# Optimization experiments

Measured on AMD Instinct MI355X. Metric: run time of the kernel, lower is better.

## Reference

```python
import jax, jax.numpy as jnp
import numpy as np

V = 50000

def _spmm(edge_vals, edge_row, edge_col, x):
    # sparse (V,V) @ dense (V,F) via gather + segment_sum
    return jax.ops.segment_sum(edge_vals[:, None] * x[edge_col], edge_row, num_segments=V)

def setup_inputs() -> dict:
    key = jax.random.key(0)
    ks = jax.random.split(key, 6)
    B, Cin, Cout, K, E = 4, 128, 128, 4, 800000
    x = jax.random.normal(ks[0], (B, Cin, V), dtype=jnp.float32)
    edge_row = jax.random.randint(ks[1], (E,), 0, V, dtype=jnp.int32)
    edge_col = jax.random.randint(ks[2], (E,), 0, V, dtype=jnp.int32)
    edge_vals = jax.random.normal(ks[3], (E,), dtype=jnp.float32) * 0.05
    std = np.sqrt(2.0 / (Cin * K)).astype(np.float32)
    weights = jax.random.normal(ks[4], (K, Cin, Cout), dtype=jnp.float32) * std
    biases = jnp.full((Cout,), 0.01, dtype=jnp.float32)
    return {"x": x, "edge_row": edge_row, "edge_col": edge_col,
            "edge_vals": edge_vals, "weights": weights, "biases": biases}

def reference(x, edge_row, edge_col, edge_vals, weights, biases):
    B, Cin, Vv = x.shape
    K = weights.shape[0]
    # (B,Cin,V) -> (V, B*Cin)
    x0 = jnp.transpose(x, (2, 0, 1)).reshape(Vv, B * Cin)
    xs = [x0]
    if K > 1:
        x1 = _spmm(edge_vals, edge_row, edge_col, x0)
        xs.append(x1)
        for _ in range(2, K):
            x2 = 2.0 * _spmm(edge_vals, edge_row, edge_col, x1) - x0
            xs.append(x2)
            x0, x1 = x1, x2
    xk = jnp.stack(xs, 0).reshape(K, Vv, B, Cin)
    # tensordot over (K, Cin): (K,V,B,Cin) x (K,Cin,Cout) -> (V,B,Cout)
    out = jnp.einsum('kvbc,kco->vbo', xk, weights)
    out = out + biases
    # permute (V,B,Cout) -> (B,Cout,V)
    return jnp.transpose(out, (1, 2, 0))
```

## Files before the change

kernel.cpp:

```cpp
#include <hip/hip_runtime.h>

#define V_N   50000
#define B_N   4
#define C_IN  128
#define C_OUT 128
#define E_N   800000
#define F_N   512
#define M_TOT 200000

typedef unsigned short ushort_t;
typedef __attribute__((ext_vector_type(8))) short short8;
typedef __attribute__((ext_vector_type(4))) float f32x4;

__device__ __forceinline__ float bf_lo(unsigned u) { return __uint_as_float(u << 16); }
__device__ __forceinline__ float bf_hi(unsigned u) { return __uint_as_float(u & 0xFFFF0000u); }
__device__ __forceinline__ ushort_t f2bf(float f) {
    unsigned u = __float_as_uint(f);
    u += 0x7FFFu + ((u >> 16) & 1u);
    return (ushort_t)(u >> 16);
}

__global__ __launch_bounds__(256) void k_transpose_in(const float* __restrict__ x,
                                                      ushort_t* __restrict__ x0) {
    __shared__ float tile[32][33];
    int vb = blockIdx.x * 32;
    int fb = blockIdx.y * 32;
    int tx = threadIdx.x, ty = threadIdx.y;
#pragma unroll
    for (int i = 0; i < 32; i += 8) {
        int f = fb + ty + i, v = vb + tx;
        float val = 0.f;
        if (v < V_N) val = x[(size_t)f * V_N + v];
        tile[ty + i][tx] = val;
    }
    __syncthreads();
#pragma unroll
    for (int i = 0; i < 32; i += 8) {
        int v = vb + ty + i, f = fb + tx;
        if (v < V_N) x0[(size_t)v * F_N + f] = f2bf(tile[tx][ty + i]);
    }
}

__global__ __launch_bounds__(256) void k_hist(const int* __restrict__ row,
                                              int* __restrict__ counts) {
    int e = blockIdx.x * blockDim.x + threadIdx.x;
    if (e < E_N) atomicAdd(&counts[row[e]], 1);
}

__global__ __launch_bounds__(1024) void k_scan(const int* __restrict__ counts,
                                               int* __restrict__ row_ptr,
                                               int* __restrict__ next) {
    __shared__ int sums[1024];
    int t = threadIdx.x;
    const int CH = (V_N + 1023) / 1024;
    int base = t * CH;
    int s = 0;
    for (int i = 0; i < CH; i++) {
        int idx = base + i;
        if (idx < V_N) s += counts[idx];
    }
    sums[t] = s;
    __syncthreads();
    for (int off = 1; off < 1024; off <<= 1) {
        int v = (t >= off) ? sums[t - off] : 0;
        __syncthreads();
        sums[t] += v;
        __syncthreads();
    }
    int run = (t == 0) ? 0 : sums[t - 1];
    for (int i = 0; i < CH; i++) {
        int idx = base + i;
        if (idx < V_N) {
            row_ptr[idx] = run;
            next[idx]    = run;
            run += counts[idx];
        }
    }
    if (t == 1023) row_ptr[V_N] = run;
}

__global__ __launch_bounds__(256) void k_scatter(const int* __restrict__ row,
                                                 const int* __restrict__ col,
                                                 const float* __restrict__ vals,
                                                 int* __restrict__ next,
                                                 int2* __restrict__ edges) {
    int e = blockIdx.x * blockDim.x + threadIdx.x;
    if (e < E_N) {
        int r = row[e];
        int pos = atomicAdd(&next[r], 1);
        edges[pos] = make_int2(col[e], __float_as_int(vals[e]));
    }
}

__global__ __launch_bounds__(256) void k_wprep(const float* __restrict__ W,
                                               ushort_t* __restrict__ Wt) {
    int i = blockIdx.x * 256 + threadIdx.x;
    int k = i >> 14, c = (i >> 7) & 127, o = i & 127;
    Wt[((size_t)k * 128 + o) * 128 + c] = f2bf(W[i]);
}

__global__ __launch_bounds__(256) void k_spmm_bf16(const int* __restrict__ row_ptr,
                                                   const int2* __restrict__ edges,
                                                   const ushort_t* __restrict__ src,
                                                   const ushort_t* __restrict__ prev,
                                                   ushort_t* __restrict__ dst,
                                                   float alpha, float beta,
                                                   int has_prev) {
    int lane = threadIdx.x & 63;
    int g = blockIdx.x * 4 + (threadIdx.x >> 6);
    int r = g >> 1;
    int h = g & 1;
    int e0 = row_ptr[r], e1 = row_ptr[r + 1];
    float a0 = 0.f, a1 = 0.f, a2 = 0.f, a3 = 0.f;
    const ushort_t* sp = src + h * 256 + lane * 4;

    int e = e0;
    for (; e + 4 <= e1; e += 4) {
        int2 E0 = edges[e], E1 = edges[e + 1], E2 = edges[e + 2], E3 = edges[e + 3];
        uint2 g0 = *(const uint2*)(sp + (size_t)E0.x * F_N);
        uint2 g1 = *(const uint2*)(sp + (size_t)E1.x * F_N);
        uint2 g2 = *(const uint2*)(sp + (size_t)E2.x * F_N);
        uint2 g3 = *(const uint2*)(sp + (size_t)E3.x * F_N);
        float w0 = __int_as_float(E0.y), w1 = __int_as_float(E1.y);
        float w2 = __int_as_float(E2.y), w3 = __int_as_float(E3.y);
        a0 += w0 * bf_lo(g0.x); a1 += w0 * bf_hi(g0.x);
        a2 += w0 * bf_lo(g0.y); a3 += w0 * bf_hi(g0.y);
        a0 += w1 * bf_lo(g1.x); a1 += w1 * bf_hi(g1.x);
        a2 += w1 * bf_lo(g1.y); a3 += w1 * bf_hi(g1.y);
        a0 += w2 * bf_lo(g2.x); a1 += w2 * bf_hi(g2.x);
        a2 += w2 * bf_lo(g2.y); a3 += w2 * bf_hi(g2.y);
        a0 += w3 * bf_lo(g3.x); a1 += w3 * bf_hi(g3.x);
        a2 += w3 * bf_lo(g3.y); a3 += w3 * bf_hi(g3.y);
    }
    for (; e < e1; e++) {
        int2 E = edges[e];
        uint2 gv = *(const uint2*)(sp + (size_t)E.x * F_N);
        float w = __int_as_float(E.y);
        a0 += w * bf_lo(gv.x); a1 += w * bf_hi(gv.x);
        a2 += w * bf_lo(gv.y); a3 += w * bf_hi(gv.y);
    }

    size_t off = (size_t)r * F_N + h * 256 + lane * 4;
    if (has_prev) {
        uint2 pv = *(const uint2*)(prev + off);
        a0 = alpha * a0 + beta * bf_lo(pv.x);
        a1 = alpha * a1 + beta * bf_hi(pv.x);
        a2 = alpha * a2 + beta * bf_lo(pv.y);
        a3 = alpha * a3 + beta * bf_hi(pv.y);
    } else {
        a0 *= alpha; a1 *= alpha; a2 *= alpha; a3 *= alpha;
    }
    ushort_t res[4] = {f2bf(a0), f2bf(a1), f2bf(a2), f2bf(a3)};
    *(uint2*)(dst + off) = *(const uint2*)res;
}

__global__ __launch_bounds__(256, 2) void k_gemm_mfma(
        const ushort_t* __restrict__ X0, const ushort_t* __restrict__ X1,
        const ushort_t* __restrict__ X2, const ushort_t* __restrict__ X3,
        const ushort_t* __restrict__ Wt, const float* __restrict__ bias,
        float* __restrict__ out) {
    __shared__ ushort_t As[128][40];
    __shared__ ushort_t Bs[128][40];
    __shared__ float    Cs[64][133];

    int tid  = threadIdx.x;
    int lane = tid & 63;
    int wave = tid >> 6;
    int wm = wave >> 1, wn = wave & 1;
    int quad = lane >> 4, l15 = lane & 15;
    int m_blk = blockIdx.x * 128;

    f32x4 acc[4][4];
#pragma unroll
    for (int fi = 0; fi < 4; fi++)
#pragma unroll
        for (int fj = 0; fj < 4; fj++) {
            acc[fi][fj][0] = 0.f; acc[fi][fj][1] = 0.f;
            acc[fi][fj][2] = 0.f; acc[fi][fj][3] = 0.f;
        }

    const ushort_t* Xb[4] = {X0, X1, X2, X3};

    for (int kb = 0; kb < 4; kb++) {
        const ushort_t* A = Xb[kb];
        const ushort_t* W = Wt + (size_t)kb * (128 * 128);
        for (int kk = 0; kk < 128; kk += 32) {
            __syncthreads();
#pragma unroll
            for (int i = 0; i < 2; i++) {
                int id = tid + i * 256;
                int rr = id >> 2, p = id & 3;
                int gm = m_blk + rr; if (gm >= M_TOT) gm = M_TOT - 1;
                *(uint4*)&As[rr][p * 8] = *(const uint4*)&A[(size_t)gm * 128 + kk + p * 8];
                *(uint4*)&Bs[rr][p * 8] = *(const uint4*)&W[(size_t)rr * 128 + kk + p * 8];
            }
            __syncthreads();
            short8 a[4], b[4];
#pragma unroll
            for (int f = 0; f < 4; f++) {
                a[f] = *(const short8*)&As[wm * 64 + f * 16 + l15][quad * 8];
                b[f] = *(const short8*)&Bs[wn * 64 + f * 16 + l15][quad * 8];
            }
#pragma unroll
            for (int fi = 0; fi < 4; fi++)
#pragma unroll
                for (int fj = 0; fj < 4; fj++)
                    acc[fi][fj] = __builtin_amdgcn_mfma_f32_16x16x32_bf16(
                        a[fi], b[fj], acc[fi][fj], 0, 0, 0);
        }
    }

    int v_blk = m_blk >> 2;
    for (int h = 0; h < 2; h++) {
        __syncthreads();
        if (wm == h) {
#pragma unroll
            for (int fi = 0; fi < 4; fi++)
#pragma unroll
                for (int fj = 0; fj < 4; fj++) {
                    int ml = fi * 16 + quad * 4;
                    int n  = wn * 64 + fj * 16 + l15;
#pragma unroll
                    for (int reg = 0; reg < 4; reg++)
                        Cs[ml + reg][n] = acc[fi][fj][reg];
                }
        }
        __syncthreads();
#pragma unroll
        for (int i = 0; i < 8; i++) {
            int idx = tid + i * 256;
            int v4  = idx & 3;
            int o   = (idx >> 2) & 127;
            int b   = idx >> 9;
            int vl  = v4 * 4;
            float bv = bias[o];
            float r0 = Cs[(vl + 0) * 4 + b][o] + bv;
            float r1 = Cs[(vl + 1) * 4 + b][o] + bv;
            float r2 = Cs[(vl + 2) * 4 + b][o] + bv;
            float r3 = Cs[(vl + 3) * 4 + b][o] + bv;
            int v0 = v_blk + h * 16 + vl;
            float* op = out + ((size_t)b * C_OUT + o) * V_N + v0;
            if (v0 + 3 < V_N) {
                *(float4*)op = make_float4(r0, r1, r2, r3);
            } else {
                if (v0     < V_N) op[0] = r0;
                if (v0 + 1 < V_N) op[1] = r1;
                if (v0 + 2 < V_N) op[2] = r2;
                if (v0 + 3 < V_N) op[3] = r3;
            }
        }
    }
}

extern "C" void kernel_launch(void* const* d_in, const int* in_sizes, int n_in,
                              void* d_out, int out_size, void* d_ws, size_t ws_size,
                              hipStream_t stream) {
    const float* x        = (const float*)d_in[0];
    const int*   edge_row = (const int*)  d_in[1];
    const int*   edge_col = (const int*)  d_in[2];
    const float* edge_val = (const float*)d_in[3];
    const float* weights  = (const float*)d_in[4];
    const float* biases   = (const float*)d_in[5];
    float* out = (float*)d_out;

    const size_t XSZ = (size_t)V_N * F_N;
    ushort_t* x0 = (ushort_t*)d_ws;
    ushort_t* x1 = x0 + XSZ;
    ushort_t* x2 = x1 + XSZ;
    ushort_t* x3 = x2 + XSZ;
    ushort_t* Wt = x3 + XSZ;
    int* iw      = (int*)(Wt + 4 * 128 * 128);
    int* row_ptr = iw;
    int* counts  = iw + 50016;
    int* nxt     = iw + 100032;
    int2* edges  = (int2*)(iw + 150048);

    dim3 tb(32, 8);
    dim3 tgrid((V_N + 31) / 32, F_N / 32);

    k_transpose_in<<<tgrid, tb, 0, stream>>>(x, x0);

    hipMemsetAsync(counts, 0, V_N * sizeof(int), stream);
    k_hist<<<(E_N + 255) / 256, 256, 0, stream>>>(edge_row, counts);
    k_scan<<<1, 1024, 0, stream>>>(counts, row_ptr, nxt);
    k_scatter<<<(E_N + 255) / 256, 256, 0, stream>>>(edge_row, edge_col, edge_val,
                                                     nxt, edges);

    k_wprep<<<256, 256, 0, stream>>>(weights, Wt);

    k_spmm_bf16<<<V_N * 2 / 4, 256, 0, stream>>>(row_ptr, edges, x0, x0, x1,
                                                 1.f, 0.f, 0);
    k_spmm_bf16<<<V_N * 2 / 4, 256, 0, stream>>>(row_ptr, edges, x1, x0, x2,
                                                 2.f, -1.f, 1);
    k_spmm_bf16<<<V_N * 2 / 4, 256, 0, stream>>>(row_ptr, edges, x2, x1, x3,
                                                 2.f, -1.f, 1);

    k_gemm_mfma<<<(M_TOT + 127) / 128, 256, 0, stream>>>(x0, x1, x2, x3, Wt,
                                                         biases, out);
}
```

Baseline: 834.7 us.

## Replace single-block row-pointer scan with multi-block three-phase scan

The exclusive prefix sum over per-row edge counts used to run in one 1024-thread block, where each thread walked a strided chunk serially. It is now split into three kernels: a per-block scan of 1024 elements with coalesced loads, a single-wavefront shuffle scan over the block totals, and a pass that adds each block's offset and fills row_ptr and next. This spreads the scan across many CUs but adds two extra kernel launches and an additional read/write pass over row_ptr.

```diff
diff --git a/kernel.cpp b/kernel.cpp
--- a/kernel.cpp
+++ b/kernel.cpp
@@ -8,6 +8,9 @@
 #define F_N   512
 #define M_TOT 200000
 
+#define SCAN_BLK  1024
+#define SCAN_NB   ((V_N + SCAN_BLK - 1) / SCAN_BLK)
+
 typedef unsigned short ushort_t;
 typedef __attribute__((ext_vector_type(8))) short short8;
 typedef __attribute__((ext_vector_type(4))) float f32x4;
@@ -47,36 +50,62 @@
     if (e < E_N) atomicAdd(&counts[row[e]], 1);
 }
 
-__global__ __launch_bounds__(1024) void k_scan(const int* __restrict__ counts,
-                                               int* __restrict__ row_ptr,
-                                               int* __restrict__ next) {
-    __shared__ int sums[1024];
+__global__ __launch_bounds__(256) void k_scan_blk(const int* __restrict__ counts,
+                                                  int* __restrict__ row_ptr,
+                                                  int* __restrict__ blk_sums) {
+    __shared__ int s[256];
     int t = threadIdx.x;
-    const int CH = (V_N + 1023) / 1024;
-    int base = t * CH;
-    int s = 0;
-    for (int i = 0; i < CH; i++) {
-        int idx = base + i;
-        if (idx < V_N) s += counts[idx];
-    }
-    sums[t] = s;
+    int base = blockIdx.x * SCAN_BLK + t * 4;
+    int c0 = (base + 0 < V_N) ? counts[base + 0] : 0;
+    int c1 = (base + 1 < V_N) ? counts[base + 1] : 0;
+    int c2 = (base + 2 < V_N) ? counts[base + 2] : 0;
+    int c3 = (base + 3 < V_N) ? counts[base + 3] : 0;
+    int p1 = c0, p2 = c0 + c1, p3 = c0 + c1 + c2, tot = p3 + c3;
+    s[t] = tot;
     __syncthreads();
-    for (int off = 1; off < 1024; off <<= 1) {
-        int v = (t >= off) ? sums[t - off] : 0;
+#pragma unroll
+    for (int off = 1; off < 256; off <<= 1) {
+        int v = (t >= off) ? s[t - off] : 0;
         __syncthreads();
-        sums[t] += v;
+        s[t] += v;
         __syncthreads();
     }
-    int run = (t == 0) ? 0 : sums[t - 1];
-    for (int i = 0; i < CH; i++) {
+    int excl = (t == 0) ? 0 : s[t - 1];
+    if (base + 0 < V_N) row_ptr[base + 0] = excl;
+    if (base + 1 < V_N) row_ptr[base + 1] = excl + p1;
+    if (base + 2 < V_N) row_ptr[base + 2] = excl + p2;
+    if (base + 3 < V_N) row_ptr[base + 3] = excl + p3;
+    if (t == 255) blk_sums[blockIdx.x] = s[255];
+}
+
+__global__ __launch_bounds__(64) void k_scan_top(const int* __restrict__ blk_sums,
+                                                 int* __restrict__ blk_off) {
+    int t = threadIdx.x;
+    int v = (t < SCAN_NB) ? blk_sums[t] : 0;
+#pragma unroll
+    for (int off = 1; off < 64; off <<= 1) {
+        int u = __shfl_up(v, off);
+        if (t >= off) v += u;
+    }
+    blk_off[t] = v;
+}
+
+__global__ __launch_bounds__(256) void k_scan_add(const int* __restrict__ blk_off,
+                                                  int* __restrict__ row_ptr,
+                                                  int* __restrict__ next) {
+    int b = blockIdx.x, t = threadIdx.x;
+    int off = (b == 0) ? 0 : blk_off[b - 1];
+    int base = b * SCAN_BLK + t * 4;
+#pragma unroll
+    for (int i = 0; i < 4; i++) {
         int idx = base + i;
         if (idx < V_N) {
-            row_ptr[idx] = run;
-            next[idx]    = run;
-            run += counts[idx];
-        }
-    }
-    if (t == 1023) row_ptr[V_N] = run;
+            int rv = row_ptr[idx] + off;
+            row_ptr[idx] = rv;
+            next[idx]    = rv;
+        }
+    }
+    if (b == 0 && t == 0) row_ptr[V_N] = blk_off[SCAN_NB - 1];
 }
 
 __global__ __launch_bounds__(256) void k_scatter(const int* __restrict__ row,
@@ -273,7 +302,9 @@
     int* row_ptr = iw;
     int* counts  = iw + 50016;
     int* nxt     = iw + 100032;
-    int2* edges  = (int2*)(iw + 150048);
+    int* blk_sums= iw + 150048;
+    int* blk_off = iw + 150112;
+    int2* edges  = (int2*)(iw + 150176);
 
     dim3 tb(32, 8);
     dim3 tgrid((V_N + 31) / 32, F_N / 32);
@@ -282,7 +313,9 @@
 
     hipMemsetAsync(counts, 0, V_N * sizeof(int), stream);
     k_hist<<<(E_N + 255) / 256, 256, 0, stream>>>(edge_row, counts);
-    k_scan<<<1, 1024, 0, stream>>>(counts, row_ptr, nxt);
+    k_scan_blk<<<SCAN_NB, 256, 0, stream>>>(counts, row_ptr, blk_sums);
+    k_scan_top<<<1, 64, 0, stream>>>(blk_sums, blk_off);
+    k_scan_add<<<SCAN_NB, 256, 0, stream>>>(blk_off, row_ptr, nxt);
     k_scatter<<<(E_N + 255) / 256, 256, 0, stream>>>(edge_row, edge_col, edge_val,
                                                      nxt, edges);
 
```

Measured after the change: 724.6 us. 13.2% less time.
